# Kernel tuning notes

Measured on AMD Instinct MI355X. Metric: run time of the kernel, lower is better.

The kernel has to match this reference:

```python
import jax, jax.numpy as jnp
import numpy as np

B, L, DIM, DIM_ATTN, NUM_HEADS = 2, 2048, 1024, 1024, 16
HEAD_DIM = DIM_ATTN // NUM_HEADS


def setup_inputs() -> dict:
    key = jax.random.key(0)
    ks = jax.random.split(key, 7)
    scale = 1.0 / np.sqrt(DIM)
    return {
        "x": jax.random.normal(ks[0], (B, L, DIM), dtype=jnp.float32),
        "mask": jax.random.randint(ks[1], (B, L), 0, 2, dtype=jnp.int32),
        "pos_bias": jax.random.normal(ks[2], (1, NUM_HEADS, L, L), dtype=jnp.float32),
        "Wq": jax.random.normal(ks[3], (DIM, DIM_ATTN), dtype=jnp.float32) * scale,
        "Wk": jax.random.normal(ks[4], (DIM, DIM_ATTN), dtype=jnp.float32) * scale,
        "Wv": jax.random.normal(ks[5], (DIM, DIM_ATTN), dtype=jnp.float32) * scale,
        "Wo": jax.random.normal(ks[6], (DIM_ATTN, DIM), dtype=jnp.float32) * scale,
    }


def reference(x, mask, pos_bias, Wq, Wk, Wv, Wo):
    Bq, L1, _ = x.shape
    n = pos_bias.shape[1]
    # self-attention: context = x
    q = (x @ Wq).reshape(Bq, L1, n, HEAD_DIM)
    k = (x @ Wk).reshape(Bq, L1, n, HEAD_DIM)
    v = (x @ Wv).reshape(Bq, L1, n, HEAD_DIM)
    # additive bias: pos_bias broadcast to (B, n, L1, L2), masked positions -> dtype min
    neg_inf = jnp.finfo(x.dtype).min
    attn_bias = jnp.where(mask[:, None, None, :] > 0, pos_bias, neg_inf)
    # unscaled T5-style scores
    attn = jnp.einsum('binc,bjnc->bnij', q, k) + attn_bias
    attn = jax.nn.softmax(attn.astype(jnp.float32), axis=-1).astype(x.dtype)
    out = jnp.einsum('bnij,bjnc->binc', attn, v).reshape(Bq, L1, n * HEAD_DIM)
    return out @ Wo
```

## Files before the change

kernel.cpp:

```cpp
#include <hip/hip_runtime.h>
#include <float.h>
#include <math.h>

typedef short s16x8 __attribute__((ext_vector_type(8)));
typedef float f32x4 __attribute__((ext_vector_type(4)));
typedef unsigned short u16t;
typedef u16t u16x4v __attribute__((ext_vector_type(4)));

__device__ __forceinline__ u16t f2bf(float f){
  unsigned u = __builtin_bit_cast(unsigned, f);
  return (u16t)((u + 0x7FFFu + ((u >> 16) & 1u)) >> 16);
}
__device__ __forceinline__ float bf2f(u16t b){
  unsigned u = ((unsigned)b) << 16;
  return __builtin_bit_cast(float, u);
}
__device__ __forceinline__ f32x4 mfma16(s16x8 a, s16x8 b, f32x4 c){
  return __builtin_amdgcn_mfma_f32_16x16x32_bf16(a, b, c, 0, 0, 0);
}

__global__ __launch_bounds__(256) void prep_split(const float* __restrict__ X,
    u16t* __restrict__ H, u16t* __restrict__ L, int n8){
  int i = blockIdx.x * 256 + threadIdx.x;
  if (i >= n8) return;
  const float* p = X + (size_t)i * 8;
  float4 a = *(const float4*)p;
  float4 b = *(const float4*)(p + 4);
  float v[8] = {a.x, a.y, a.z, a.w, b.x, b.y, b.z, b.w};
  s16x8 hv, lv;
#pragma unroll
  for (int r = 0; r < 8; ++r){
    u16t hh = f2bf(v[r]);
    hv[r] = (short)hh;
    lv[r] = (short)f2bf(v[r] - bf2f(hh));
  }
  *(s16x8*)(H + (size_t)i * 8) = hv;
  *(s16x8*)(L + (size_t)i * 8) = lv;
}

__global__ __launch_bounds__(256) void prep_wt(
    const float* __restrict__ Wq, const float* __restrict__ Wk,
    const float* __restrict__ Wv, const float* __restrict__ Wo,
    u16t* __restrict__ Qh, u16t* __restrict__ Ql,
    u16t* __restrict__ Kh, u16t* __restrict__ Kl,
    u16t* __restrict__ Vh,
    u16t* __restrict__ Oh, u16t* __restrict__ Ol){
  __shared__ float T[64][65];
  int z = blockIdx.z;
  const float* W = (z==0)?Wq:(z==1)?Wk:(z==2)?Wv:Wo;
  u16t* OH = (z==0)?Qh:(z==1)?Kh:(z==2)?Vh:Oh;
  u16t* OL = (z==0)?Ql:(z==1)?Kl:(z==2)?(u16t*)0:Ol;
  int k0 = blockIdx.x*64, n0 = blockIdx.y*64;
  int r = threadIdx.x >> 2, c = (threadIdx.x & 3) * 16;
#pragma unroll
  for (int i = 0; i < 4; ++i){
    float4 v = *(const float4*)&W[(size_t)(k0 + r)*1024 + n0 + c + i*4];
    T[r][c + i*4 + 0] = v.x; T[r][c + i*4 + 1] = v.y;
    T[r][c + i*4 + 2] = v.z; T[r][c + i*4 + 3] = v.w;
  }
  __syncthreads();
  s16x8 hv0, hv1, lv0, lv1;
#pragma unroll
  for (int i = 0; i < 16; ++i){
    float v = T[c + i][r];
    u16t hh = f2bf(v);
    u16t ll = f2bf(v - bf2f(hh));
    if (i < 8){ hv0[i] = (short)hh; lv0[i] = (short)ll; }
    else      { hv1[i-8] = (short)hh; lv1[i-8] = (short)ll; }
  }
  size_t o = (size_t)(n0 + r)*1024 + k0 + c;
  *(s16x8*)(OH + o)     = hv0;
  *(s16x8*)(OH + o + 8) = hv1;
  if (OL){ *(s16x8*)(OL + o) = lv0; *(s16x8*)(OL + o + 8) = lv1; }
}

template<int NSPLIT, int MODE>
__global__ __launch_bounds__(256) void gemm_k(
    const u16t* __restrict__ Agh, const u16t* __restrict__ Agl,
    const u16t* __restrict__ Bgh0, const u16t* __restrict__ Bgl0,
    const u16t* __restrict__ Bgh1, const u16t* __restrict__ Bgl1,
    u16t* __restrict__ Oh0, u16t* __restrict__ Ol0,
    u16t* __restrict__ Oh1, u16t* __restrict__ Ol1,
    float* __restrict__ Of)
{
  constexpr int NPLANES = (NSPLIT==3) ? 4 : 2;
  __shared__ u16t SM[NPLANES * 4096];
  u16t* AH = SM;
  u16t* AL = SM + 4096;
  u16t* BH = SM + ((NSPLIT==3) ? 8192 : 4096);
  u16t* BL = SM + 12288;

  const u16t* Bgh = blockIdx.z ? Bgh1 : Bgh0;
  const u16t* Bgl = blockIdx.z ? Bgl1 : Bgl0;
  u16t* Oh = blockIdx.z ? Oh1 : Oh0;
  u16t* Ol = blockIdx.z ? Ol1 : Ol0;

  const int t = threadIdx.x;
  const int lane = t & 63;
  const int wid = t >> 6;
  const int wm = wid >> 1, wn = wid & 1;
  const int bm = blockIdx.x * 128, bn = blockIdx.y * 128;
  const int li = lane & 15, lg = lane >> 4;

  f32x4 acc[4][4];
#pragma unroll
  for (int i = 0; i < 4; ++i)
#pragma unroll
    for (int j = 0; j < 4; ++j) acc[i][j] = f32x4{0.f, 0.f, 0.f, 0.f};

  for (int k0 = 0; k0 < 1024; k0 += 32){
    __syncthreads();
#pragma unroll
    for (int i = 0; i < 2; ++i){
      int cch = i*256 + t;
      int row = cch >> 2, sl = cch & 3;
      int sw = (sl ^ ((row >> 1) & 3)) * 8;
      *(s16x8*)&AH[row*32 + sw] = *(const s16x8*)&Agh[(size_t)(bm+row)*1024 + k0 + sl*8];
      if constexpr (NSPLIT == 3)
        *(s16x8*)&AL[row*32 + sw] = *(const s16x8*)&Agl[(size_t)(bm+row)*1024 + k0 + sl*8];
      *(s16x8*)&BH[row*32 + sw] = *(const s16x8*)&Bgh[(size_t)(bn+row)*1024 + k0 + sl*8];
      if constexpr (NSPLIT == 3)
        *(s16x8*)&BL[row*32 + sw] = *(const s16x8*)&Bgl[(size_t)(bn+row)*1024 + k0 + sl*8];
    }
    __syncthreads();

    s16x8 ah[4], alv[4], bh[4], blv[4];
#pragma unroll
    for (int i = 0; i < 4; ++i){
      int rowA = wm*64 + i*16 + li;
      int swA = (lg ^ ((rowA >> 1) & 3)) * 8;
      ah[i] = *(const s16x8*)&AH[rowA*32 + swA];
      if constexpr (NSPLIT == 3) alv[i] = *(const s16x8*)&AL[rowA*32 + swA];
      int rowB = wn*64 + i*16 + li;
      int swB = (lg ^ ((rowB >> 1) & 3)) * 8;
      bh[i] = *(const s16x8*)&BH[rowB*32 + swB];
      if constexpr (NSPLIT == 3) blv[i] = *(const s16x8*)&BL[rowB*32 + swB];
    }
#pragma unroll
    for (int i = 0; i < 4; ++i)
#pragma unroll
      for (int j = 0; j < 4; ++j){
        acc[i][j] = mfma16(ah[i], bh[j], acc[i][j]);
        if constexpr (NSPLIT == 3){
          acc[i][j] = mfma16(ah[i], blv[j], acc[i][j]);
          acc[i][j] = mfma16(alv[i], bh[j], acc[i][j]);
        }
      }
  }

#pragma unroll
  for (int i = 0; i < 4; ++i)
#pragma unroll
    for (int j = 0; j < 4; ++j){
      if constexpr (MODE == 1){
        int n = bn + wn*64 + j*16 + li;
        int tok0 = bm + wm*64 + i*16 + lg*4;
        u16x4v pk;
#pragma unroll
        for (int r = 0; r < 4; ++r) pk[r] = f2bf(acc[i][j][r]);
        *(u16x4v*)&Oh[(size_t)n*4096 + tok0] = pk;
      } else {
#pragma unroll
        for (int r = 0; r < 4; ++r){
          int tok = bm + wm*64 + i*16 + lg*4 + r;
          int col = bn + wn*64 + j*16 + li;
          float v = acc[i][j][r];
          if constexpr (MODE == 0){
            u16t hh = f2bf(v);
            Oh[(size_t)tok*1024 + col] = hh;
            Ol[(size_t)tok*1024 + col] = f2bf(v - bf2f(hh));
          } else {
            Of[(size_t)tok*1024 + col] = v;
          }
        }
      }
    }
}

__global__ __launch_bounds__(256) void attn_mfma(
    const u16t* __restrict__ Qh, const u16t* __restrict__ Ql,
    const u16t* __restrict__ Kh, const u16t* __restrict__ Kl,
    const u16t* __restrict__ Vt, const float* __restrict__ bias,
    const int* __restrict__ mask,
    u16t* __restrict__ Ah, u16t* __restrict__ Al)
{
  __shared__ u16t SM[6 * 4096];
  __shared__ u16t PL[4][16 * 72];

  const int t = threadIdx.x, lane = t & 63, wid = t >> 6;
  const int h = blockIdx.y;
  const int q0 = blockIdx.x * 64;
  const int lg = lane >> 4, li = lane & 15;
  const int qrow = q0 + wid*16 + li;

  s16x8 qf[2][2][2];
#pragma unroll
  for (int b = 0; b < 2; ++b)
#pragma unroll
    for (int c = 0; c < 2; ++c){
      size_t o = (size_t)(b*2048 + qrow)*1024 + h*64 + c*32 + lg*8;
      qf[b][c][0] = *(const s16x8*)&Qh[o];
      qf[b][c][1] = *(const s16x8*)&Ql[o];
    }

  f32x4 Oacc[2][4];
#pragma unroll
  for (int b = 0; b < 2; ++b)
#pragma unroll
    for (int d = 0; d < 4; ++d) Oacc[b][d] = f32x4{0.f,0.f,0.f,0.f};
  float m_s[2] = {-__builtin_inff(), -__builtin_inff()};
  float l_s[2] = {0.f, 0.f};

  for (int k0 = 0; k0 < 2048; k0 += 64){
    __syncthreads();
#pragma unroll
    for (int p = 0; p < 6; ++p){
      int b = (p >= 3) ? 1 : 0, kind = p - b*3;
#pragma unroll
      for (int i = 0; i < 2; ++i){
        int cch = i*256 + t;
        int row = cch >> 3, sl = cch & 7;
        const u16t* src;
        if (kind == 0)      src = &Kh[(size_t)(b*2048 + k0 + row)*1024 + h*64 + sl*8];
        else if (kind == 1) src = &Kl[(size_t)(b*2048 + k0 + row)*1024 + h*64 + sl*8];
        else                src = &Vt[(size_t)(h*64 + row)*4096 + b*2048 + k0 + sl*8];
        *(s16x8*)&SM[p*4096 + row*64 + ((sl ^ (row & 7)) * 8)] = *(const s16x8*)src;
      }
    }
    __syncthreads();

#pragma unroll
    for (int b = 0; b < 2; ++b){
      const u16t* KHL = SM + (b*3+0)*4096;
      const u16t* KLL = SM + (b*3+1)*4096;
      const u16t* VTL = SM + (b*3+2)*4096;

      f32x4 sa[4];
#pragma unroll
      for (int tt = 0; tt < 4; ++tt) sa[tt] = f32x4{0.f,0.f,0.f,0.f};
#pragma unroll
      for (int tt = 0; tt < 4; ++tt)
#pragma unroll
        for (int c = 0; c < 2; ++c){
          int row = tt*16 + li;
          int off = row*64 + (((c*4 + lg) ^ (row & 7)) * 8);
          s16x8 kh = *(const s16x8*)&KHL[off];
          s16x8 kl = *(const s16x8*)&KLL[off];
          sa[tt] = mfma16(kh, qf[b][c][0], sa[tt]);
          sa[tt] = mfma16(kh, qf[b][c][1], sa[tt]);
          sa[tt] = mfma16(kl, qf[b][c][0], sa[tt]);
        }

      float pv[4][4];
      float rm = -FLT_MAX;
#pragma unroll
      for (int tt = 0; tt < 4; ++tt){
        float4 bb = *(const float4*)&bias[(size_t)(h*2048 + qrow)*2048 + k0 + tt*16 + lg*4];
        int4 mk = *(const int4*)&mask[b*2048 + k0 + tt*16 + lg*4];
        float ba[4] = {bb.x, bb.y, bb.z, bb.w};
        int ma[4] = {mk.x, mk.y, mk.z, mk.w};
#pragma unroll
        for (int r = 0; r < 4; ++r){
          float s = (ma[r] > 0) ? sa[tt][r] + ba[r] : -FLT_MAX;
          pv[tt][r] = s;
          rm = fmaxf(rm, s);
        }
      }
      rm = fmaxf(rm, __shfl_xor(rm, 16, 64));
      rm = fmaxf(rm, __shfl_xor(rm, 32, 64));
      float mo = m_s[b];
      float mn = fmaxf(mo, rm);
      float sc = __expf(mo - mn);
      float rs = 0.f;
#pragma unroll
      for (int tt = 0; tt < 4; ++tt)
#pragma unroll
        for (int r = 0; r < 4; ++r){
          float p = __expf(pv[tt][r] - mn);
          pv[tt][r] = p;
          rs += p;
        }
      rs += __shfl_xor(rs, 16, 64);
      rs += __shfl_xor(rs, 32, 64);
      m_s[b] = mn;
      l_s[b] = l_s[b]*sc + rs;

#pragma unroll
      for (int tt = 0; tt < 4; ++tt){
        u16x4v pk;
#pragma unroll
        for (int r = 0; r < 4; ++r) pk[r] = f2bf(pv[tt][r]);
        *(u16x4v*)&PL[wid][li*72 + tt*16 + lg*4] = pk;
      }

      float scb[4];
#pragma unroll
      for (int r = 0; r < 4; ++r) scb[r] = __shfl(sc, lg*4 + r, 64);
#pragma unroll
      for (int d = 0; d < 4; ++d)
#pragma unroll
        for (int r = 0; r < 4; ++r) Oacc[b][d][r] *= scb[r];

      s16x8 pf[2];
#pragma unroll
      for (int c = 0; c < 2; ++c)
        pf[c] = *(const s16x8*)&PL[wid][li*72 + c*32 + lg*8];
#pragma unroll
      for (int d = 0; d < 4; ++d)
#pragma unroll
        for (int c = 0; c < 2; ++c){
          int row = d*16 + li;
          s16x8 vf = *(const s16x8*)&VTL[row*64 + (((c*4 + lg) ^ (row & 7)) * 8)];
          Oacc[b][d] = mfma16(pf[c], vf, Oacc[b][d]);
        }
    }
  }

#pragma unroll
  for (int b = 0; b < 2; ++b){
    float inv[4];
#pragma unroll
    for (int r = 0; r < 4; ++r){
      float lr = __shfl(l_s[b], lg*4 + r, 64);
      inv[r] = 1.f / lr;
    }
#pragma unroll
    for (int d = 0; d < 4; ++d)
#pragma unroll
      for (int r = 0; r < 4; ++r){
        size_t tok = (size_t)(b*2048 + q0 + wid*16 + lg*4 + r);
        int col = h*64 + d*16 + li;
        float v = Oacc[b][d][r] * inv[r];
        u16t hh = f2bf(v);
        Ah[tok*1024 + col] = hh;
        Al[tok*1024 + col] = f2bf(v - bf2f(hh));
      }
  }
}

extern "C" void kernel_launch(void* const* d_in, const int* in_sizes, int n_in,
                              void* d_out, int out_size, void* d_ws, size_t ws_size,
                              hipStream_t stream)
{
  (void)in_sizes; (void)n_in; (void)out_size; (void)ws_size;
  const float* x    = (const float*)d_in[0];
  const int*   mask = (const int*)d_in[1];
  const float* bias = (const float*)d_in[2];
  const float* Wq   = (const float*)d_in[3];
  const float* Wk   = (const float*)d_in[4];
  const float* Wv   = (const float*)d_in[5];
  const float* Wo   = (const float*)d_in[6];
  float* out = (float*)d_out;

  uint8_t* wsb = (uint8_t*)d_ws;
  const size_t MB = (size_t)1 << 20;
  u16t* Xh   = (u16t*)(wsb +  0*MB);
  u16t* Xl   = (u16t*)(wsb +  8*MB);
  u16t* Wqth = (u16t*)(wsb + 16*MB);
  u16t* Wqtl = (u16t*)(wsb + 18*MB);
  u16t* Wkth = (u16t*)(wsb + 20*MB);
  u16t* Wktl = (u16t*)(wsb + 22*MB);
  u16t* Wvth = (u16t*)(wsb + 24*MB);
  u16t* Woth = (u16t*)(wsb + 26*MB);
  u16t* Wotl = (u16t*)(wsb + 28*MB);
  u16t* Qh_  = (u16t*)(wsb + 30*MB);
  u16t* Ql_  = (u16t*)(wsb + 38*MB);
  u16t* Kh_  = (u16t*)(wsb + 46*MB);
  u16t* Kl_  = (u16t*)(wsb + 54*MB);
  u16t* Vt_  = (u16t*)(wsb + 16*MB);
  u16t* Aath = Xh;
  u16t* Aatl = Xl;

  prep_split<<<dim3(2048), 256, 0, stream>>>(x, Xh, Xl, 4096*1024/8);
  prep_wt<<<dim3(16,16,4), 256, 0, stream>>>(Wq, Wk, Wv, Wo,
      Wqth, Wqtl, Wkth, Wktl, Wvth, Woth, Wotl);

  gemm_k<3,0><<<dim3(32,8,2), 256, 0, stream>>>(Xh, Xl, Wqth, Wqtl, Wkth, Wktl,
      Qh_, Ql_, Kh_, Kl_, nullptr);
  gemm_k<1,1><<<dim3(32,8,1), 256, 0, stream>>>(Xh, nullptr, Wvth, nullptr,
      nullptr, nullptr, Vt_, nullptr, nullptr, nullptr, nullptr);

  attn_mfma<<<dim3(32,16), 256, 0, stream>>>(Qh_, Ql_, Kh_, Kl_, Vt_, bias, mask,
      Aath, Aatl);

  gemm_k<3,2><<<dim3(32,8,1), 256, 0, stream>>>(Aath, Aatl, Woth, Wotl,
      nullptr, nullptr, nullptr, nullptr, nullptr, nullptr, out);
}
```

Baseline: 681.0 us.

## Load K/V fragments directly from global memory, dropping LDS staging in attention

Removes the shared-memory staging of Kh/Kl/Vt tiles and the two block barriers per key tile, so each wave loads its MFMA operand fragments straight from global memory. The bias loads are hoisted out of the batch loop and issued up front, and launch bounds ask for 3 blocks per CU. This trades LDS traffic and synchronisation for redundant global/L2 reads, since all four waves now fetch the same K/V data, plus less coalesced access patterns.

```diff
diff --git a/kernel.cpp b/kernel.cpp
--- a/kernel.cpp
+++ b/kernel.cpp
@@ -177,14 +177,13 @@
     }
 }
 
-__global__ __launch_bounds__(256) void attn_mfma(
+__global__ __launch_bounds__(256, 3) void attn_mfma(
     const u16t* __restrict__ Qh, const u16t* __restrict__ Ql,
     const u16t* __restrict__ Kh, const u16t* __restrict__ Kl,
     const u16t* __restrict__ Vt, const float* __restrict__ bias,
     const int* __restrict__ mask,
     u16t* __restrict__ Ah, u16t* __restrict__ Al)
 {
-  __shared__ u16t SM[6 * 4096];
   __shared__ u16t PL[4][16 * 72];
 
   const int t = threadIdx.x, lane = t & 63, wid = t >> 6;
@@ -212,29 +211,13 @@
   float l_s[2] = {0.f, 0.f};
 
   for (int k0 = 0; k0 < 2048; k0 += 64){
-    __syncthreads();
-#pragma unroll
-    for (int p = 0; p < 6; ++p){
-      int b = (p >= 3) ? 1 : 0, kind = p - b*3;
-#pragma unroll
-      for (int i = 0; i < 2; ++i){
-        int cch = i*256 + t;
-        int row = cch >> 3, sl = cch & 7;
-        const u16t* src;
-        if (kind == 0)      src = &Kh[(size_t)(b*2048 + k0 + row)*1024 + h*64 + sl*8];
-        else if (kind == 1) src = &Kl[(size_t)(b*2048 + k0 + row)*1024 + h*64 + sl*8];
-        else                src = &Vt[(size_t)(h*64 + row)*4096 + b*2048 + k0 + sl*8];
-        *(s16x8*)&SM[p*4096 + row*64 + ((sl ^ (row & 7)) * 8)] = *(const s16x8*)src;
-      }
-    }
-    __syncthreads();
+    float4 bb[4];
+#pragma unroll
+    for (int tt = 0; tt < 4; ++tt)
+      bb[tt] = *(const float4*)&bias[(size_t)(h*2048 + qrow)*2048 + k0 + tt*16 + lg*4];
 
 #pragma unroll
     for (int b = 0; b < 2; ++b){
-      const u16t* KHL = SM + (b*3+0)*4096;
-      const u16t* KLL = SM + (b*3+1)*4096;
-      const u16t* VTL = SM + (b*3+2)*4096;
-
       f32x4 sa[4];
 #pragma unroll
       for (int tt = 0; tt < 4; ++tt) sa[tt] = f32x4{0.f,0.f,0.f,0.f};
@@ -242,10 +225,9 @@
       for (int tt = 0; tt < 4; ++tt)
 #pragma unroll
         for (int c = 0; c < 2; ++c){
-          int row = tt*16 + li;
-          int off = row*64 + (((c*4 + lg) ^ (row & 7)) * 8);
-          s16x8 kh = *(const s16x8*)&KHL[off];
-          s16x8 kl = *(const s16x8*)&KLL[off];
+          size_t ko = (size_t)(b*2048 + k0 + tt*16 + li)*1024 + h*64 + c*32 + lg*8;
+          s16x8 kh = *(const s16x8*)&Kh[ko];
+          s16x8 kl = *(const s16x8*)&Kl[ko];
           sa[tt] = mfma16(kh, qf[b][c][0], sa[tt]);
           sa[tt] = mfma16(kh, qf[b][c][1], sa[tt]);
           sa[tt] = mfma16(kl, qf[b][c][0], sa[tt]);
@@ -255,9 +237,8 @@
       float rm = -FLT_MAX;
 #pragma unroll
       for (int tt = 0; tt < 4; ++tt){
-        float4 bb = *(const float4*)&bias[(size_t)(h*2048 + qrow)*2048 + k0 + tt*16 + lg*4];
         int4 mk = *(const int4*)&mask[b*2048 + k0 + tt*16 + lg*4];
-        float ba[4] = {bb.x, bb.y, bb.z, bb.w};
+        float ba[4] = {bb[tt].x, bb[tt].y, bb[tt].z, bb[tt].w};
         int ma[4] = {mk.x, mk.y, mk.z, mk.w};
 #pragma unroll
         for (int r = 0; r < 4; ++r){
@@ -309,8 +290,8 @@
       for (int d = 0; d < 4; ++d)
 #pragma unroll
         for (int c = 0; c < 2; ++c){
-          int row = d*16 + li;
-          s16x8 vf = *(const s16x8*)&VTL[row*64 + (((c*4 + lg) ^ (row & 7)) * 8)];
+          size_t vo = (size_t)(h*64 + d*16 + li)*4096 + b*2048 + k0 + c*32 + lg*8;
+          s16x8 vf = *(const s16x8*)&Vt[vo];
           Oacc[b][d] = mfma16(pf[c], vf, Oacc[b][d]);
         }
     }
```

After: 926.5 us. 36.0% more time.
